# Kernel tuning notes

Hardware: AMD Instinct MI355X
Metric: run time of the kernel (lower is better)

The kernel has to match this reference:

```python
import jax, jax.numpy as jnp
import numpy as np

HIDDEN = 768
HEADS = 12
HEAD_DIM = HIDDEN // HEADS


def setup_inputs() -> dict:
    key = jax.random.key(0)
    ks = jax.random.split(key, 9)
    B, S = 2, 2048
    scale = 1.0 / np.sqrt(HIDDEN)
    return {
        "hidden_states": jax.random.normal(ks[0], (B, S, HIDDEN), jnp.float32),
        "context": jax.random.normal(ks[1], (B, S, HIDDEN), jnp.float32),
        "attention_mask": jnp.zeros((B, 1, 1, S), jnp.float32),
        "Wq": jax.random.normal(ks[2], (HIDDEN, HIDDEN), jnp.float32) * scale,
        "bq": jnp.zeros((HIDDEN,), jnp.float32),
        "Wk": jax.random.normal(ks[3], (HIDDEN, HIDDEN), jnp.float32) * scale,
        "bk": jnp.zeros((HIDDEN,), jnp.float32),
        "Wv": jax.random.normal(ks[4], (HIDDEN, HIDDEN), jnp.float32) * scale,
        "bv": jnp.zeros((HIDDEN,), jnp.float32),
    }


def _split_heads(x):
    # [B, S, H*D] -> [B, H, S, D]
    B, S, _ = x.shape
    return x.reshape(B, S, HEADS, HEAD_DIM).transpose(0, 2, 1, 3)


def reference(hidden_states, context, attention_mask, Wq, bq, Wk, bk, Wv, bv):
    # torch Linear: y = x @ W^T + b
    q = _split_heads(hidden_states @ Wq.T + bq)   # [B,H,Sq,D]
    k = _split_heads(context @ Wk.T + bk)         # [B,H,Sk,D]
    v = _split_heads(context @ Wv.T + bv)         # [B,H,Sk,D]

    scores = jnp.einsum("bhqd,bhkd->bhqk", q, k)
    scores = scores / np.sqrt(HEAD_DIM + 1e-05)
    scores = scores + attention_mask
    probs = jax.nn.softmax(scores, axis=-1)       # dropout p=0 -> identity (eval)
    ctx = jnp.einsum("bhqk,bhkd->bhqd", probs, v) # [B,H,Sq,D]
    B, H, Sq, D = ctx.shape
    return ctx.transpose(0, 2, 1, 3).reshape(B, Sq, H * D)
```

## Files before the change

### kernel.cpp

```cpp
#include <hip/hip_runtime.h>
#include <hip/hip_bf16.h>
#include <math.h>

typedef short s16x8 __attribute__((ext_vector_type(8)));
typedef float f32x4 __attribute__((ext_vector_type(4)));
typedef _Float16 f16x4 __attribute__((ext_vector_type(4)));
typedef __fp16 fp16x2 __attribute__((ext_vector_type(2)));
typedef unsigned short u16;

#define NHEADS 12
#define SEQ 2048
#define NBH 24
#define KDIM 768
#define LOG2E 1.44269504088896f

#define SWZ(row, col) (((row) * 64) + ((col) ^ (((row) & 7) << 3)))

#define GLOAD_LDS16(g, l) __builtin_amdgcn_global_load_lds( \
    (const __attribute__((address_space(1))) unsigned int*)(g), \
    (__attribute__((address_space(3))) unsigned int*)(l), 16, 0, 0)

static __device__ __forceinline__ u16 f2bf(float f) {
    union { float f; unsigned u; } v; v.f = f;
    unsigned r = v.u + 0x7fffu + ((v.u >> 16) & 1u);
    return (u16)(r >> 16);
}
static __device__ __forceinline__ u16 f2h(float f) {
    union { _Float16 h; u16 u; } v; v.h = (_Float16)f;
    return v.u;
}
static __device__ __forceinline__ f16x4 pack4(float a, float b, float c, float d) {
    union { fp16x2 h2[2]; f16x4 h4; } u;
    u.h2[0] = __builtin_amdgcn_cvt_pkrtz(a, b);
    u.h2[1] = __builtin_amdgcn_cvt_pkrtz(c, d);
    return u.h4;
}

__global__ void cvt6_kernel(const float* __restrict__ s0, const float* __restrict__ s1,
                            const float* __restrict__ s2, const float* __restrict__ s3,
                            const float* __restrict__ s4, const float* __restrict__ s5,
                            u16* __restrict__ d0, u16* __restrict__ d1, u16* __restrict__ d2,
                            u16* __restrict__ d3, u16* __restrict__ d4, float* __restrict__ d5,
                            int n4a, int n4w, float qscl) {
    const int z = blockIdx.z;
    int i = blockIdx.x * blockDim.x + threadIdx.x;
    if (z == 5) {
        if (i < (2 * SEQ) / 4) {
            float4 f = ((const float4*)s5)[i];
            f.x *= LOG2E; f.y *= LOG2E; f.z *= LOG2E; f.w *= LOG2E;
            ((float4*)d5)[i] = f;
        }
        return;
    }
    const float* src = (z == 0) ? s0 : (z == 1) ? s1 : (z == 2) ? s2 : (z == 3) ? s3 : s4;
    u16* dst         = (z == 0) ? d0 : (z == 1) ? d1 : (z == 2) ? d2 : (z == 3) ? d3 : d4;
    const int n4     = (z < 2) ? n4a : n4w;
    const float scl  = (z == 2) ? qscl : 1.0f;
    if (i < n4) {
        float4 f = ((const float4*)src)[i];
        ushort4 o;
        o.x = f2bf(f.x * scl); o.y = f2bf(f.y * scl); o.z = f2bf(f.z * scl); o.w = f2bf(f.w * scl);
        ((ushort4*)dst)[i] = o;
    }
}

__launch_bounds__(256)
__global__ void qkv_gemm(const u16* __restrict__ X, const u16* __restrict__ C,
                         const u16* __restrict__ W0, const u16* __restrict__ W1, const u16* __restrict__ W2,
                         const float* __restrict__ b0, const float* __restrict__ b1, const float* __restrict__ b2,
                         u16* __restrict__ Qo, u16* __restrict__ Ko, u16* __restrict__ Vo, float qscl) {
    const int z = blockIdx.z;
    const u16* A    = (z == 0) ? X  : C;
    const u16* W    = (z == 0) ? W0 : (z == 1) ? W1 : W2;
    const float* bi = (z == 0) ? b0 : (z == 1) ? b1 : b2;
    u16* out        = (z == 0) ? Qo : (z == 1) ? Ko : Vo;
    const float bscl = (z == 0) ? qscl : 1.0f;

    __shared__ u16 As[2][128 * 64];
    __shared__ u16 Bs[2][128 * 64];

    const int tid  = threadIdx.x;
    const int lane = tid & 63;
    const int wid  = tid >> 6;
    const int wr = wid >> 1, wc = wid & 1;
    const int l15 = lane & 15, lh = lane >> 4;
    const int mBase = blockIdx.x * 128;
    const int nBase = blockIdx.y * 128;

    size_t aSrc[4], bSrc[4]; int ldsOffG[4];
    #pragma unroll
    for (int i = 0; i < 4; ++i) {
        int L = wid * 512 + i * 2048 + lane * 8;
        int row = L >> 6;
        int col = (L & 63) ^ ((row & 7) << 3);
        aSrc[i] = (size_t)(mBase + row) * KDIM + col;
        bSrc[i] = (size_t)(nBase + row) * KDIM + col;
        ldsOffG[i] = wid * 512 + i * 2048;
    }

    f32x4 acc[4][4] = {};

    #pragma unroll
    for (int i = 0; i < 4; ++i) {
        GLOAD_LDS16(&A[aSrc[i]], &As[0][ldsOffG[i]]);
        GLOAD_LDS16(&W[bSrc[i]], &Bs[0][ldsOffG[i]]);
    }

    const int NIT = KDIM / 64;
    for (int it = 0; it < NIT; ++it) {
        const int cur = it & 1;
        __syncthreads();
        if (it + 1 < NIT) {
            const int kb = (it + 1) * 64;
            #pragma unroll
            for (int i = 0; i < 4; ++i) {
                GLOAD_LDS16(&A[aSrc[i] + kb], &As[cur ^ 1][ldsOffG[i]]);
                GLOAD_LDS16(&W[bSrc[i] + kb], &Bs[cur ^ 1][ldsOffG[i]]);
            }
        }
        #pragma unroll
        for (int kk = 0; kk < 2; ++kk) {
            s16x8 xf[4], wf[4];
            #pragma unroll
            for (int m = 0; m < 4; ++m)
                xf[m] = *(const s16x8*)(&As[cur][SWZ(wr * 64 + m * 16 + l15, kk * 32 + lh * 8)]);
            #pragma unroll
            for (int n = 0; n < 4; ++n)
                wf[n] = *(const s16x8*)(&Bs[cur][SWZ(wc * 64 + n * 16 + l15, kk * 32 + lh * 8)]);
            if (z < 2) {
                #pragma unroll
                for (int m = 0; m < 4; ++m)
                    #pragma unroll
                    for (int n = 0; n < 4; ++n)
                        acc[m][n] = __builtin_amdgcn_mfma_f32_16x16x32_bf16(wf[n], xf[m], acc[m][n], 0, 0, 0);
            } else {
                #pragma unroll
                for (int m = 0; m < 4; ++m)
                    #pragma unroll
                    for (int n = 0; n < 4; ++n)
                        acc[m][n] = __builtin_amdgcn_mfma_f32_16x16x32_bf16(xf[m], wf[n], acc[m][n], 0, 0, 0);
            }
        }
    }

    if (z < 2) {
        #pragma unroll
        for (int m = 0; m < 4; ++m) {
            int sg = mBase + wr * 64 + m * 16 + l15;
            int b = sg >> 11, s = sg & 2047;
            #pragma unroll
            for (int n = 0; n < 4; ++n) {
                int d0 = nBase + wc * 64 + n * 16 + lh * 4;
                int h = d0 >> 6, d = d0 & 63;
                float4 bv = *(const float4*)(&bi[d0]);
                ushort4 o;
                o.x = f2bf(acc[m][n][0] + bv.x * bscl);
                o.y = f2bf(acc[m][n][1] + bv.y * bscl);
                o.z = f2bf(acc[m][n][2] + bv.z * bscl);
                o.w = f2bf(acc[m][n][3] + bv.w * bscl);
                *(ushort4*)(&out[(((size_t)(b * NHEADS + h) * SEQ + s) << 6) + d]) = o;
            }
        }
    } else {
        #pragma unroll
        for (int m = 0; m < 4; ++m) {
            #pragma unroll
            for (int n = 0; n < 4; ++n) {
                int colg = nBase + wc * 64 + n * 16 + l15;
                float bv = bi[colg];
                int h = colg >> 6, d = colg & 63;
                int rowg0 = mBase + wr * 64 + m * 16 + lh * 4;
                int b = rowg0 >> 11, s = rowg0 & 2047;
                int sp = (s & ~0x3C) | (((s >> 2) & 3) << 4) | (((s >> 4) & 3) << 2);
                ushort4 o;
                o.x = f2h(acc[m][n][0] + bv);
                o.y = f2h(acc[m][n][1] + bv);
                o.z = f2h(acc[m][n][2] + bv);
                o.w = f2h(acc[m][n][3] + bv);
                *(ushort4*)(&out[(((size_t)(b * NHEADS + h) * 64 + d) << 11) + sp]) = o;
            }
        }
    }
}

template<bool SPLIT>
__launch_bounds__(512)
__global__ void attn_kernel(const u16* __restrict__ Qg, const u16* __restrict__ Kg,
                            const u16* __restrict__ Vg,
                            const float* __restrict__ maskL, float* __restrict__ out,
                            float* __restrict__ Opart, float* __restrict__ MLpart) {
    __shared__ u16 Ks[2][64 * 64];
    __shared__ u16 Vt[2][64 * 64];
    __shared__ float maskLds[2048];

    const int tid  = threadIdx.x;
    const int lane = tid & 63;
    const int wid  = tid >> 6;
    const int bh = blockIdx.y;
    const int b = bh / NHEADS;
    const int h = bh % NHEADS;
    const int q0 = blockIdx.x * 128 + wid * 16;
    const int l15 = lane & 15, lh = lane >> 4;
    const int z = SPLIT ? blockIdx.z : 0;
    const int NT = SPLIT ? (SEQ / 128) : (SEQ / 64);
    const int tile0 = z * NT;

    for (int i = tid * 4; i < NT * 64; i += 512 * 4)
        *(float4*)(&maskLds[i]) = *(const float4*)(&maskL[(size_t)b * SEQ + (tile0 << 6) + i]);

    const int srow = tid >> 3;
    const int scol = ((tid & 7) * 8) ^ ((srow & 7) << 3);
    const size_t kSrc = (((size_t)bh * SEQ + srow) << 6) + scol + ((size_t)tile0 << 12);
    const size_t vSrc = (((size_t)bh * 64 + srow) << 11) + scol + (size_t)tile0 * 64;
    const int ldsBase = wid * 512;

    s16x8 qf[2];
    #pragma unroll
    for (int kk = 0; kk < 2; ++kk)
        qf[kk] = *(const s16x8*)(&Qg[(((size_t)bh * SEQ + q0 + l15) << 6) + kk * 32 + lh * 8]);

    f32x4 oacc[4] = {};
    float mrun = -1e30f, lrun = 0.f;

    GLOAD_LDS16(&Kg[kSrc], &Ks[0][ldsBase]);
    GLOAD_LDS16(&Vg[vSrc], &Vt[0][ldsBase]);

    for (int t = 0; t < NT; ++t) {
        const int cur = t & 1;
        __syncthreads();
        if (t + 1 < NT) {
            GLOAD_LDS16(&Kg[kSrc + ((size_t)(t + 1) << 12)], &Ks[cur ^ 1][ldsBase]);
            GLOAD_LDS16(&Vg[vSrc + (size_t)(t + 1) * 64],    &Vt[cur ^ 1][ldsBase]);
        }

        f32x4 sacc[4];
        #pragma unroll
        for (int n = 0; n < 4; ++n) {
            float4 mv = *(const float4*)(&maskLds[t * 64 + n * 16 + lh * 4]);
            sacc[n][0] = mv.x; sacc[n][1] = mv.y; sacc[n][2] = mv.z; sacc[n][3] = mv.w;
        }
        __builtin_amdgcn_s_setprio(1);
        #pragma unroll
        for (int kk = 0; kk < 2; ++kk) {
            #pragma unroll
            for (int n = 0; n < 4; ++n) {
                s16x8 kf = *(const s16x8*)(&Ks[cur][SWZ(n * 16 + l15, kk * 32 + lh * 8)]);
                sacc[n] = __builtin_amdgcn_mfma_f32_16x16x32_bf16(kf, qf[kk], sacc[n], 0, 0, 0);
            }
        }
        __builtin_amdgcn_s_setprio(0);

        float tmax = sacc[0][0];
        #pragma unroll
        for (int n = 0; n < 4; ++n)
            #pragma unroll
            for (int j = 0; j < 4; ++j)
                tmax = fmaxf(tmax, sacc[n][j]);

        if (!__all(tmax - mrun <= 11.0f)) {
            float rmax = fmaxf(tmax, __shfl_xor(tmax, 16));
            rmax = fmaxf(rmax, __shfl_xor(rmax, 32));
            float mnew = fmaxf(mrun, rmax);
            float alpha = __builtin_amdgcn_exp2f(mrun - mnew);
            lrun *= alpha;
            #pragma unroll
            for (int nd = 0; nd < 4; ++nd)
                #pragma unroll
                for (int j = 0; j < 4; ++j)
                    oacc[nd][j] *= alpha;
            mrun = mnew;
        }

        f16x4 pf[4];
        #pragma unroll
        for (int n = 0; n < 4; ++n) {
            float p0 = __builtin_amdgcn_exp2f(sacc[n][0] - mrun);
            float p1 = __builtin_amdgcn_exp2f(sacc[n][1] - mrun);
            float p2 = __builtin_amdgcn_exp2f(sacc[n][2] - mrun);
            float p3 = __builtin_amdgcn_exp2f(sacc[n][3] - mrun);
            lrun += (p0 + p1) + (p2 + p3);
            pf[n] = pack4(p0, p1, p2, p3);
        }

        __builtin_amdgcn_s_setprio(1);
        #pragma unroll
        for (int kk = 0; kk < 2; ++kk) {
            #pragma unroll
            for (int nd = 0; nd < 4; ++nd) {
                s16x8 v2 = *(const s16x8*)(&Vt[cur][SWZ(nd * 16 + l15, lh * 16 + kk * 8)]);
                union { s16x8 s8; f16x4 h4[2]; } u; u.s8 = v2;
                oacc[nd] = __builtin_amdgcn_mfma_f32_16x16x16f16(u.h4[0], pf[2 * kk],     oacc[nd], 0, 0, 0);
                oacc[nd] = __builtin_amdgcn_mfma_f32_16x16x16f16(u.h4[1], pf[2 * kk + 1], oacc[nd], 0, 0, 0);
            }
        }
        __builtin_amdgcn_s_setprio(0);
    }

    lrun += __shfl_xor(lrun, 16);
    lrun += __shfl_xor(lrun, 32);

    const float inv = 1.0f / lrun;
    const int s = q0 + l15;
    if (!SPLIT) {
        #pragma unroll
        for (int nd = 0; nd < 4; ++nd) {
            float4 o;
            o.x = oacc[nd][0] * inv; o.y = oacc[nd][1] * inv;
            o.z = oacc[nd][2] * inv; o.w = oacc[nd][3] * inv;
            *(float4*)(&out[(size_t)(b * SEQ + s) * (NHEADS * 64) + h * 64 + nd * 16 + lh * 4]) = o;
        }
    } else {
        const size_t rbase = ((size_t)(z * NBH + bh) * SEQ + s);
        #pragma unroll
        for (int nd = 0; nd < 4; ++nd) {
            float4 o;
            o.x = oacc[nd][0] * inv; o.y = oacc[nd][1] * inv;
            o.z = oacc[nd][2] * inv; o.w = oacc[nd][3] * inv;
            *(float4*)(&Opart[rbase * 64 + nd * 16 + lh * 4]) = o;
        }
        if (lh == 0)
            *(float2*)(&MLpart[rbase * 2]) = make_float2(mrun, lrun);
    }
}

__global__ void combine_kernel(const float* __restrict__ Opart, const float* __restrict__ MLpart,
                               float* __restrict__ out) {
    int gid = blockIdx.x * 256 + threadIdx.x;
    int row = gid >> 4, d4 = gid & 15;
    float2 ml0 = ((const float2*)MLpart)[row];
    float2 ml1 = ((const float2*)MLpart)[NBH * SEQ + row];
    float m = fmaxf(ml0.x, ml1.x);
    float w0 = __builtin_amdgcn_exp2f(ml0.x - m) * ml0.y;
    float w1 = __builtin_amdgcn_exp2f(ml1.x - m) * ml1.y;
    float inv = 1.0f / (w0 + w1);
    w0 *= inv; w1 *= inv;
    float4 o0 = *(const float4*)(&Opart[(size_t)row * 64 + d4 * 4]);
    float4 o1 = *(const float4*)(&Opart[(size_t)NBH * SEQ * 64 + (size_t)row * 64 + d4 * 4]);
    float4 o;
    o.x = o0.x * w0 + o1.x * w1; o.y = o0.y * w0 + o1.y * w1;
    o.z = o0.z * w0 + o1.z * w1; o.w = o0.w * w0 + o1.w * w1;
    int bh = row >> 11, s = row & 2047;
    int b = bh / NHEADS, hh = bh % NHEADS;
    *(float4*)(&out[(size_t)(b * SEQ + s) * (NHEADS * 64) + hh * 64 + d4 * 4]) = o;
}

extern "C" void kernel_launch(void* const* d_in, const int* in_sizes, int n_in,
                              void* d_out, int out_size, void* d_ws, size_t ws_size,
                              hipStream_t stream) {
    const float* hidden  = (const float*)d_in[0];
    const float* context = (const float*)d_in[1];
    const float* mask    = (const float*)d_in[2];
    const float* Wq = (const float*)d_in[3];
    const float* bq = (const float*)d_in[4];
    const float* Wk = (const float*)d_in[5];
    const float* bk = (const float*)d_in[6];
    const float* Wv = (const float*)d_in[7];
    const float* bv = (const float*)d_in[8];
    float* out = (float*)d_out;

    char* ws = (char*)d_ws;
    const size_t XSZ = (size_t)4096 * 768 * 2;
    const size_t WSZ = (size_t)768 * 768 * 2;
    u16* X16  = (u16*)(ws);
    u16* C16  = (u16*)(ws + XSZ);
    u16* W16q = (u16*)(ws + 2 * XSZ);
    u16* W16k = (u16*)(ws + 2 * XSZ + WSZ);
    u16* W16v = (u16*)(ws + 2 * XSZ + 2 * WSZ);
    u16* Q16  = (u16*)(ws + 2 * XSZ + 3 * WSZ);
    u16* K16  = (u16*)(ws + 3 * XSZ + 3 * WSZ);
    u16* V16  = (u16*)(ws + 4 * XSZ + 3 * WSZ);
    const size_t MASKL_OFF = 5 * XSZ + 3 * WSZ;
    float* maskL = (float*)(ws + MASKL_OFF);
    const size_t OPART_OFF = MASKL_OFF + 2 * SEQ * sizeof(float) + 256;
    float* Opart = (float*)(ws + OPART_OFF);
    const size_t ML_OFF = OPART_OFF + (size_t)2 * NBH * SEQ * 64 * 4;
    float* MLpart = (float*)(ws + ML_OFF);
    const size_t WS_NEED_SPLIT = ML_OFF + (size_t)2 * NBH * SEQ * 2 * 4;

    const float qscl = (float)((1.0 / sqrt(64.0 + 1e-5)) * 1.44269504088896);

    const int n4x = 4096 * 768 / 4;
    const int n4w = 768 * 768 / 4;
    cvt6_kernel<<<dim3((n4x + 255) / 256, 1, 6), 256, 0, stream>>>(
        hidden, context, Wq, Wk, Wv, mask,
        X16, C16, W16q, W16k, W16v, maskL, n4x, n4w, qscl);

    qkv_gemm<<<dim3(4096 / 128, 768 / 128, 3), 256, 0, stream>>>(
        X16, C16, W16q, W16k, W16v, bq, bk, bv, Q16, K16, V16, qscl);

    if (ws_size >= WS_NEED_SPLIT) {
        attn_kernel<true><<<dim3(SEQ / 128, NBH, 2), 512, 0, stream>>>(
            Q16, K16, V16, maskL, out, Opart, MLpart);
        combine_kernel<<<(NBH * SEQ * 16) / 256, 256, 0, stream>>>(Opart, MLpart, out);
    } else {
        attn_kernel<false><<<dim3(SEQ / 128, NBH, 1), 512, 0, stream>>>(
            Q16, K16, V16, maskL, out, Opart, MLpart);
    }
}
```

Measured before the change: 93.03 us.

## Shrink GEMM K-tile to 32 and store split-attention partials in fp16

```diff
diff --git a/kernel.cpp b/kernel.cpp
--- a/kernel.cpp
+++ b/kernel.cpp
@@ -15,6 +15,7 @@
 #define LOG2E 1.44269504088896f
 
 #define SWZ(row, col) (((row) * 64) + ((col) ^ (((row) & 7) << 3)))
+#define SWZ32(row, col) (((row) * 32) + ((col) ^ (((row) & 3) << 3)))
 
 #define GLOAD_LDS16(g, l) __builtin_amdgcn_global_load_lds( \
     (const __attribute__((address_space(1))) unsigned int*)(g), \
@@ -64,7 +65,7 @@
     }
 }
 
-__launch_bounds__(256)
+__launch_bounds__(256, 4)
 __global__ void qkv_gemm(const u16* __restrict__ X, const u16* __restrict__ C,
                          const u16* __restrict__ W0, const u16* __restrict__ W1, const u16* __restrict__ W2,
                          const float* __restrict__ b0, const float* __restrict__ b1, const float* __restrict__ b2,
@@ -76,8 +77,8 @@
     u16* out        = (z == 0) ? Qo : (z == 1) ? Ko : Vo;
     const float bscl = (z == 0) ? qscl : 1.0f;
 
-    __shared__ u16 As[2][128 * 64];
-    __shared__ u16 Bs[2][128 * 64];
+    __shared__ u16 As[2][128 * 32];
+    __shared__ u16 Bs[2][128 * 32];
 
     const int tid  = threadIdx.x;
     const int lane = tid & 63;
@@ -87,12 +88,12 @@
     const int mBase = blockIdx.x * 128;
     const int nBase = blockIdx.y * 128;
 
-    size_t aSrc[4], bSrc[4]; int ldsOffG[4];
+    size_t aSrc[2], bSrc[2]; int ldsOffG[2];
     #pragma unroll
-    for (int i = 0; i < 4; ++i) {
-        int L = wid * 512 + i * 2048 + lane * 8;
-        int row = L >> 6;
-        int col = (L & 63) ^ ((row & 7) << 3);
+    for (int i = 0; i < 2; ++i) {
+        int L = tid * 8 + i * 2048;
+        int row = L >> 5;
+        int col = (L & 31) ^ ((row & 3) << 3);
         aSrc[i] = (size_t)(mBase + row) * KDIM + col;
         bSrc[i] = (size_t)(nBase + row) * KDIM + col;
         ldsOffG[i] = wid * 512 + i * 2048;
@@ -101,45 +102,42 @@
     f32x4 acc[4][4] = {};
 
     #pragma unroll
-    for (int i = 0; i < 4; ++i) {
+    for (int i = 0; i < 2; ++i) {
         GLOAD_LDS16(&A[aSrc[i]], &As[0][ldsOffG[i]]);
         GLOAD_LDS16(&W[bSrc[i]], &Bs[0][ldsOffG[i]]);
     }
 
-    const int NIT = KDIM / 64;
+    const int NIT = KDIM / 32;
     for (int it = 0; it < NIT; ++it) {
         const int cur = it & 1;
         __syncthreads();
         if (it + 1 < NIT) {
-            const int kb = (it + 1) * 64;
-            #pragma unroll
-            for (int i = 0; i < 4; ++i) {
+            const int kb = (it + 1) * 32;
+            #pragma unroll
+            for (int i = 0; i < 2; ++i) {
                 GLOAD_LDS16(&A[aSrc[i] + kb], &As[cur ^ 1][ldsOffG[i]]);
                 GLOAD_LDS16(&W[bSrc[i] + kb], &Bs[cur ^ 1][ldsOffG[i]]);
             }
         }
-        #pragma unroll
-        for (int kk = 0; kk < 2; ++kk) {
-            s16x8 xf[4], wf[4];
+        s16x8 xf[4], wf[4];
+        #pragma unroll
+        for (int m = 0; m < 4; ++m)
+            xf[m] = *(const s16x8*)(&As[cur][SWZ32(wr * 64 + m * 16 + l15, lh * 8)]);
+        #pragma unroll
+        for (int n = 0; n < 4; ++n)
+            wf[n] = *(const s16x8*)(&Bs[cur][SWZ32(wc * 64 + n * 16 + l15, lh * 8)]);
+        if (z < 2) {
             #pragma unroll
             for (int m = 0; m < 4; ++m)
-                xf[m] = *(const s16x8*)(&As[cur][SWZ(wr * 64 + m * 16 + l15, kk * 32 + lh * 8)]);
-            #pragma unroll
-            for (int n = 0; n < 4; ++n)
-                wf[n] = *(const s16x8*)(&Bs[cur][SWZ(wc * 64 + n * 16 + l15, kk * 32 + lh * 8)]);
-            if (z < 2) {
                 #pragma unroll
-                for (int m = 0; m < 4; ++m)
-                    #pragma unroll
-                    for (int n = 0; n < 4; ++n)
-                        acc[m][n] = __builtin_amdgcn_mfma_f32_16x16x32_bf16(wf[n], xf[m], acc[m][n], 0, 0, 0);
-            } else {
+                for (int n = 0; n < 4; ++n)
+                    acc[m][n] = __builtin_amdgcn_mfma_f32_16x16x32_bf16(wf[n], xf[m], acc[m][n], 0, 0, 0);
+        } else {
+            #pragma unroll
+            for (int m = 0; m < 4; ++m)
                 #pragma unroll
-                for (int m = 0; m < 4; ++m)
-                    #pragma unroll
-                    for (int n = 0; n < 4; ++n)
-                        acc[m][n] = __builtin_amdgcn_mfma_f32_16x16x32_bf16(xf[m], wf[n], acc[m][n], 0, 0, 0);
-            }
+                for (int n = 0; n < 4; ++n)
+                    acc[m][n] = __builtin_amdgcn_mfma_f32_16x16x32_bf16(xf[m], wf[n], acc[m][n], 0, 0, 0);
         }
     }
 
@@ -188,7 +186,7 @@
 __global__ void attn_kernel(const u16* __restrict__ Qg, const u16* __restrict__ Kg,
                             const u16* __restrict__ Vg,
                             const float* __restrict__ maskL, float* __restrict__ out,
-                            float* __restrict__ Opart, float* __restrict__ MLpart) {
+                            u16* __restrict__ OpartH, float* __restrict__ MLpart) {
     __shared__ u16 Ks[2][64 * 64];
     __shared__ u16 Vt[2][64 * 64];
     __shared__ float maskLds[2048];
@@ -313,17 +311,17 @@
         const size_t rbase = ((size_t)(z * NBH + bh) * SEQ + s);
         #pragma unroll
         for (int nd = 0; nd < 4; ++nd) {
-            float4 o;
-            o.x = oacc[nd][0] * inv; o.y = oacc[nd][1] * inv;
-            o.z = oacc[nd][2] * inv; o.w = oacc[nd][3] * inv;
-            *(float4*)(&Opart[rbase * 64 + nd * 16 + lh * 4]) = o;
+            union { f16x4 h4; ushort4 u4; } o;
+            o.h4 = pack4(oacc[nd][0] * inv, oacc[nd][1] * inv,
+                         oacc[nd][2] * inv, oacc[nd][3] * inv);
+            *(ushort4*)(&OpartH[rbase * 64 + nd * 16 + lh * 4]) = o.u4;
         }
         if (lh == 0)
             *(float2*)(&MLpart[rbase * 2]) = make_float2(mrun, lrun);
     }
 }
 
-__global__ void combine_kernel(const float* __restrict__ Opart, const float* __restrict__ MLpart,
+__global__ void combine_kernel(const u16* __restrict__ OpartH, const float* __restrict__ MLpart,
                                float* __restrict__ out) {
     int gid = blockIdx.x * 256 + threadIdx.x;
     int row = gid >> 4, d4 = gid & 15;
@@ -334,11 +332,14 @@
     float w1 = __builtin_amdgcn_exp2f(ml1.x - m) * ml1.y;
     float inv = 1.0f / (w0 + w1);
     w0 *= inv; w1 *= inv;
-    float4 o0 = *(const float4*)(&Opart[(size_t)row * 64 + d4 * 4]);
-    float4 o1 = *(const float4*)(&Opart[(size_t)NBH * SEQ * 64 + (size_t)row * 64 + d4 * 4]);
+    union { ushort4 u4; f16x4 h4; } a, c;
+    a.u4 = *(const ushort4*)(&OpartH[(size_t)row * 64 + d4 * 4]);
+    c.u4 = *(const ushort4*)(&OpartH[(size_t)NBH * SEQ * 64 + (size_t)row * 64 + d4 * 4]);
     float4 o;
-    o.x = o0.x * w0 + o1.x * w1; o.y = o0.y * w0 + o1.y * w1;
-    o.z = o0.z * w0 + o1.z * w1; o.w = o0.w * w0 + o1.w * w1;
+    o.x = (float)a.h4[0] * w0 + (float)c.h4[0] * w1;
+    o.y = (float)a.h4[1] * w0 + (float)c.h4[1] * w1;
+    o.z = (float)a.h4[2] * w0 + (float)c.h4[2] * w1;
+    o.w = (float)a.h4[3] * w0 + (float)c.h4[3] * w1;
     int bh = row >> 11, s = row & 2047;
     int b = bh / NHEADS, hh = bh % NHEADS;
     *(float4*)(&out[(size_t)(b * SEQ + s) * (NHEADS * 64) + hh * 64 + d4 * 4]) = o;
@@ -372,8 +373,8 @@
     const size_t MASKL_OFF = 5 * XSZ + 3 * WSZ;
     float* maskL = (float*)(ws + MASKL_OFF);
     const size_t OPART_OFF = MASKL_OFF + 2 * SEQ * sizeof(float) + 256;
-    float* Opart = (float*)(ws + OPART_OFF);
-    const size_t ML_OFF = OPART_OFF + (size_t)2 * NBH * SEQ * 64 * 4;
+    u16* OpartH = (u16*)(ws + OPART_OFF);
+    const size_t ML_OFF = OPART_OFF + (size_t)2 * NBH * SEQ * 64 * 2;
     float* MLpart = (float*)(ws + ML_OFF);
     const size_t WS_NEED_SPLIT = ML_OFF + (size_t)2 * NBH * SEQ * 2 * 4;
 
@@ -390,10 +391,10 @@
 
     if (ws_size >= WS_NEED_SPLIT) {
         attn_kernel<true><<<dim3(SEQ / 128, NBH, 2), 512, 0, stream>>>(
-            Q16, K16, V16, maskL, out, Opart, MLpart);
-        combine_kernel<<<(NBH * SEQ * 16) / 256, 256, 0, stream>>>(Opart, MLpart, out);
+            Q16, K16, V16, maskL, out, OpartH, MLpart);
+        combine_kernel<<<(NBH * SEQ * 16) / 256, 256, 0, stream>>>(OpartH, MLpart, out);
     } else {
         attn_kernel<false><<<dim3(SEQ / 128, NBH, 1), 512, 0, stream>>>(
-            Q16, K16, V16, maskL, out, Opart, MLpart);
-    }
-}
+            Q16, K16, V16, maskL, out, OpartH, MLpart);
+    }
+}
```

Result: slower. 238.9 us (+156.8%).
